# Kernel optimization log

Measured on AMD Instinct MI355X. Metric: run time of the kernel, lower is better.

Reference implementation:

```python
import jax, jax.numpy as jnp
import numpy as np

NHB = 7   # spatial filter size
UF = 4    # upscale factor (PixelShuffle)
PAD = (NHB - 1) // 2


def _extract_patches(xc):
    """xc: [B,T,H,W] -> [B, T*NHB*NHB, H, W]; tap order (t, kh, kw) matching
    the identity-kernel conv3d in DynFilter3D (eye reshaped t-major)."""
    B, T, H, W = xc.shape
    xp = jnp.pad(xc, ((0, 0), (0, 0), (PAD, PAD), (PAD, PAD)))
    shifts = [xp[:, :, i:i + H, j:j + W] for i in range(NHB) for j in range(NHB)]
    p = jnp.stack(shifts, axis=2)          # [B,T,49,H,W]
    return p.reshape(B, T * NHB * NHB, H, W)


def _pixel_shuffle(t, r=UF):
    """t: [B, C*r*r, H, W] -> [B, C, H*r, W*r] (torch PixelShuffle semantics)."""
    B, C, H, W = t.shape
    oc = C // (r * r)
    t = t.reshape(B, oc, r, r, H, W)
    t = t.transpose(0, 1, 4, 2, 5, 3)      # [B,oc,H,r,W,r]
    return t.reshape(B, oc, H * r, W * r)


def setup_inputs() -> dict:
    key = jax.random.key(0)
    k1, k2 = jax.random.split(key)
    B, T, H, W = 2, 7, 128, 128
    x = jax.random.normal(k1, (B, 3, T, H, W), dtype=jnp.float32)
    # per-pixel dynamic filter logits: [B, taps=T*7*7, uf^2, H, W]
    filt = jax.random.normal(k2, (B, T * NHB * NHB, UF * UF, H, W), dtype=jnp.float32)
    return {"x": x, "filt": filt}


def reference(x, filt):
    # softmax over the 343 filter taps (FR_52L's final softmax over dim=1)
    fw = jax.nn.softmax(filt, axis=1)                      # [B,343,16,H,W]
    outs = []
    for c in range(3):                                     # fixed color channels
        p = _extract_patches(x[:, c])                      # [B,343,H,W]
        t = jnp.einsum('bphw,bpuhw->buhw', p, fw)          # per-pixel [1,343]x[343,16]
        outs.append(_pixel_shuffle(t))                     # [B,1,4H,4W]
    return jnp.concatenate(outs, axis=1)                   # [B,3,4H,4W]
```

## Files before the change

kernel.cpp:

```cpp
#include <hip/hip_runtime.h>

#define NHB   7
#define TT    7
#define HH    128
#define WW    128
#define BB    2
#define NU    16
#define NTAPS (TT * NHB * NHB)
#define NG    (TT * NHB)
#define WT    64
#define XSW   (WT + 6)
#define XSWP  72

typedef float vf2 __attribute__((ext_vector_type(2)));

__global__ __launch_bounds__(512, 4)
void dynfilt_kernel(const float* __restrict__ x,
                    const float* __restrict__ filt,
                    float* __restrict__ out) {
    __shared__ float xs[3][TT][NHB][XSWP];

    const int b     = blockIdx.z;
    const int h     = blockIdx.y;
    const int wbase = blockIdx.x * WT;

    const int tid = threadIdx.y * 32 + threadIdx.x;
    for (int i = tid; i < 3 * TT * NHB * XSW; i += 512) {
        int wl   = i % XSW;
        int rest = i / XSW;
        int r    = rest % NHB; rest /= NHB;
        int t    = rest % TT;
        int c    = rest / TT;
        int gh = h + r - 3;
        int gw = wbase + wl - 3;
        float v = 0.0f;
        if (gh >= 0 && gh < HH && gw >= 0 && gw < WW)
            v = x[((((size_t)b * 3 + c) * TT + t) * HH + gh) * WW + gw];
        xs[c][t][r][wl] = v;
    }
    __syncthreads();

    const int tx = threadIdx.x;
    const int u  = threadIdx.y;
    const int w0 = wbase + 2 * tx;

    const vf2* fp = (const vf2*)
        (filt + ((((size_t)b * NTAPS) * NU + u) * HH + h) * WW + w0);
    const size_t TAPSTRIDE2 = (size_t)NU * HH * WW / 2;

    float acc00 = 0.f, acc01 = 0.f;
    float acc10 = 0.f, acc11 = 0.f;
    float acc20 = 0.f, acc21 = 0.f;
    float den0  = 0.f, den1  = 0.f;

    const float* xbase = &xs[0][0][0][0] + 2 * tx;

    auto load_group = [&](vf2* buf) {
        #pragma unroll
        for (int kw = 0; kw < NHB; ++kw) {
            buf[kw] = __builtin_nontemporal_load(fp);
            fp += TAPSTRIDE2;
        }
    };

    auto consume = [&](const vf2* buf, int g) {
        float xr[3][8];
        #pragma unroll
        for (int c = 0; c < 3; ++c) {
            const float2* pp = (const float2*)(xbase + (c * NG + g) * XSWP);
            float2 v0 = pp[0], v1 = pp[1], v2 = pp[2], v3 = pp[3];
            xr[c][0] = v0.x; xr[c][1] = v0.y;
            xr[c][2] = v1.x; xr[c][3] = v1.y;
            xr[c][4] = v2.x; xr[c][5] = v2.y;
            xr[c][6] = v3.x; xr[c][7] = v3.y;
        }
        #pragma unroll
        for (int kw = 0; kw < NHB; ++kw) {
            float e0 = __expf(buf[kw].x);
            float e1 = __expf(buf[kw].y);
            den0 += e0; den1 += e1;
            acc00 += e0 * xr[0][kw];  acc01 += e1 * xr[0][kw + 1];
            acc10 += e0 * xr[1][kw];  acc11 += e1 * xr[1][kw + 1];
            acc20 += e0 * xr[2][kw];  acc21 += e1 * xr[2][kw + 1];
        }
    };

    vf2 bufA[NHB], bufB[NHB];
    load_group(bufA);
    load_group(bufB);
    for (int gp = 0; gp < 24; ++gp) {
        const int g = 2 * gp;
        consume(bufA, g);
        if (g + 2 < NG) load_group(bufA);
        consume(bufB, g + 1);
        if (g + 3 < NG) load_group(bufB);
    }
    consume(bufA, NG - 1);

    const float inv0 = 1.0f / den0;
    const float inv1 = 1.0f / den1;

    const int r1 = u >> 2, r2 = u & 3;
    const int oh = h * 4 + r1;
    const float res[3][2] = {
        { acc00 * inv0, acc01 * inv1 },
        { acc10 * inv0, acc11 * inv1 },
        { acc20 * inv0, acc21 * inv1 },
    };
    #pragma unroll
    for (int c = 0; c < 3; ++c) {
        size_t o = (((size_t)(b * 3 + c)) * (HH * 4) + oh) * (size_t)(WW * 4);
        out[o + (size_t)w0 * 4 + r2]       = res[c][0];
        out[o + (size_t)(w0 + 1) * 4 + r2] = res[c][1];
    }
}

extern "C" void kernel_launch(void* const* d_in, const int* in_sizes, int n_in,
                              void* d_out, int out_size, void* d_ws, size_t ws_size,
                              hipStream_t stream) {
    const float* x    = (const float*)d_in[0];
    const float* filt = (const float*)d_in[1];
    float* out        = (float*)d_out;

    dim3 grid(WW / WT, HH, BB);
    dim3 block(32, NU);
    dynfilt_kernel<<<grid, block, 0, stream>>>(x, filt, out);
}
```

Before: 863.3 us.

## Stream filter logits via async global_load_lds into double-buffered shared memory

Replaces per-thread register prefetch of the filter logits with direct global-to-LDS 16-byte async loads into a two-slot shared buffer. Each stage covers one (t,kh) group of seven taps, and manual vmcnt/lgkmcnt waits plus barriers pipeline the staging against compute. This is meant to widen memory transactions and free registers spent on prefetch buffers. In exchange it adds barriers every half-iteration and uses more LDS, so launch bounds drop to 2 blocks per SM and occupancy may fall.

```diff
diff --git a/kernel.cpp b/kernel.cpp
--- a/kernel.cpp
+++ b/kernel.cpp
@@ -1,4 +1,5 @@
 #include <hip/hip_runtime.h>
+#include <stdint.h>
 
 #define NHB   7
 #define TT    7
@@ -11,20 +12,29 @@
 #define WT    64
 #define XSW   (WT + 6)
 #define XSWP  72
+#define PLANE (NU * HH * WW)
+#define SLOTF (NHB * NU * WT)
 
-typedef float vf2 __attribute__((ext_vector_type(2)));
+__device__ __forceinline__ void gload16(const float* src, float* dst) {
+    __builtin_amdgcn_global_load_lds(
+        (const __attribute__((address_space(1))) void*)src,
+        (__attribute__((address_space(3))) void*)dst,
+        16, 0, 0);
+}
 
-__global__ __launch_bounds__(512, 4)
+__global__ __launch_bounds__(512, 2)
 void dynfilt_kernel(const float* __restrict__ x,
                     const float* __restrict__ filt,
-                    float* __restrict__ out) {
-    __shared__ float xs[3][TT][NHB][XSWP];
+                    float* __restrict__ out)
+{
+    __shared__ __align__(16) float xs[3][TT][NHB][XSWP];
+    __shared__ __align__(16) float fls[2][SLOTF];
 
     const int b     = blockIdx.z;
     const int h     = blockIdx.y;
     const int wbase = blockIdx.x * WT;
+    const int tid   = threadIdx.y * 32 + threadIdx.x;
 
-    const int tid = threadIdx.y * 32 + threadIdx.x;
     for (int i = tid; i < 3 * TT * NHB * XSW; i += 512) {
         int wl   = i % XSW;
         int rest = i / XSW;
@@ -38,15 +48,36 @@
             v = x[((((size_t)b * 3 + c) * TT + t) * HH + gh) * WW + gw];
         xs[c][t][r][wl] = v;
     }
+
+    const float* fb0 = filt + (size_t)b * NTAPS * PLANE;
+    unsigned srcoff[4];
+#pragma unroll
+    for (int j = 0; j < 4; ++j) {
+        const int k  = tid + 512 * j;
+        const int q  = k >> 8;
+        const int rr = k & 255;
+        srcoff[j] = (unsigned)q * PLANE + (unsigned)(rr >> 4) * (HH * WW)
+                  + (unsigned)h * WW + (unsigned)wbase + (unsigned)(rr & 15) * 4;
+    }
+    float* lwave = &fls[0][0] + (tid >> 6) * 256;
+
     __syncthreads();
+
+    auto stage = [&](int gg, int s) {
+        const float* fg = fb0 + (size_t)gg * (NHB * PLANE);
+        float* ld = lwave + s * SLOTF;
+        gload16(fg + srcoff[0], ld);
+        gload16(fg + srcoff[1], ld + 2048);
+        gload16(fg + srcoff[2], ld + 4096);
+        if (tid < 256) gload16(fg + srcoff[3], ld + 6144);
+    };
+
+    stage(0, 0);
+    stage(1, 1);
 
     const int tx = threadIdx.x;
     const int u  = threadIdx.y;
     const int w0 = wbase + 2 * tx;
-
-    const vf2* fp = (const vf2*)
-        (filt + ((((size_t)b * NTAPS) * NU + u) * HH + h) * WW + w0);
-    const size_t TAPSTRIDE2 = (size_t)NU * HH * WW / 2;
 
     float acc00 = 0.f, acc01 = 0.f;
     float acc10 = 0.f, acc11 = 0.f;
@@ -54,18 +85,15 @@
     float den0  = 0.f, den1  = 0.f;
 
     const float* xbase = &xs[0][0][0][0] + 2 * tx;
+    const float* fbr   = &fls[0][0] + u * WT + 2 * tx;
 
-    auto load_group = [&](vf2* buf) {
-        #pragma unroll
-        for (int kw = 0; kw < NHB; ++kw) {
-            buf[kw] = __builtin_nontemporal_load(fp);
-            fp += TAPSTRIDE2;
-        }
-    };
-
-    auto consume = [&](const vf2* buf, int g) {
+    auto consume = [&](int g, int s) {
+        const float2* fp2 = (const float2*)(fbr + s * SLOTF);
+        float2 f[NHB];
+#pragma unroll
+        for (int q = 0; q < NHB; ++q) f[q] = fp2[q * (NU * WT / 2)];
         float xr[3][8];
-        #pragma unroll
+#pragma unroll
         for (int c = 0; c < 3; ++c) {
             const float2* pp = (const float2*)(xbase + (c * NG + g) * XSWP);
             float2 v0 = pp[0], v1 = pp[1], v2 = pp[2], v3 = pp[3];
@@ -74,10 +102,10 @@
             xr[c][4] = v2.x; xr[c][5] = v2.y;
             xr[c][6] = v3.x; xr[c][7] = v3.y;
         }
-        #pragma unroll
+#pragma unroll
         for (int kw = 0; kw < NHB; ++kw) {
-            float e0 = __expf(buf[kw].x);
-            float e1 = __expf(buf[kw].y);
+            float e0 = __expf(f[kw].x);
+            float e1 = __expf(f[kw].y);
             den0 += e0; den1 += e1;
             acc00 += e0 * xr[0][kw];  acc01 += e1 * xr[0][kw + 1];
             acc10 += e0 * xr[1][kw];  acc11 += e1 * xr[1][kw + 1];
@@ -85,17 +113,24 @@
         }
     };
 
-    vf2 bufA[NHB], bufB[NHB];
-    load_group(bufA);
-    load_group(bufB);
+#define WAIT_VM3  asm volatile("s_waitcnt vmcnt(3)" ::: "memory")
+#define WAIT_VM0  asm volatile("s_waitcnt vmcnt(0)" ::: "memory")
+#define WAIT_LGKM asm volatile("s_waitcnt lgkmcnt(0)" ::: "memory")
+#define BAR       __builtin_amdgcn_s_barrier()
+
     for (int gp = 0; gp < 24; ++gp) {
         const int g = 2 * gp;
-        consume(bufA, g);
-        if (g + 2 < NG) load_group(bufA);
-        consume(bufB, g + 1);
-        if (g + 3 < NG) load_group(bufB);
+        WAIT_VM3; BAR;
+        consume(g, 0);
+        WAIT_LGKM; BAR;
+        stage(g + 2, 0);
+        WAIT_VM3; BAR;
+        consume(g + 1, 1);
+        WAIT_LGKM; BAR;
+        if (g + 3 < NG) stage(g + 3, 1);
     }
-    consume(bufA, NG - 1);
+    WAIT_VM0; BAR;
+    consume(NG - 1, 0);
 
     const float inv0 = 1.0f / den0;
     const float inv1 = 1.0f / den1;
@@ -107,7 +142,7 @@
         { acc10 * inv0, acc11 * inv1 },
         { acc20 * inv0, acc21 * inv1 },
     };
-    #pragma unroll
+#pragma unroll
     for (int c = 0; c < 3; ++c) {
         size_t o = (((size_t)(b * 3 + c)) * (HH * 4) + oh) * (size_t)(WW * 4);
         out[o + (size_t)w0 * 4 + r2]       = res[c][0];
```

Result: slower. 920.1 us (+6.6%).
